# Kernel tuning notes

Measured on AMD Instinct MI355X. Metric: run time of the kernel, lower is better.

## Reference

```python
import jax, jax.numpy as jnp
import numpy as np

IN_SHAPE = 640
LEVELS = [3, 4, 5]          # pyramid_levels [3,5] expanded
REG_LEN = 64
NUM_CLASSES = 80
MAX_OUT = 100
SCORE_TH = 0.3
IOU_TH = 0.5
NEG_INF = -1e30


def _make_anchors():
    """Anchor-free anchors: one box per grid cell, grid_zero_start=True,
    anchor_scale=1, aspect_ratio=1 -> half-size = stride/2. Normalized by input size."""
    all_a = []
    for lvl in LEVELS:
        stride = 2 ** lvl
        fs = IN_SHAPE // stride
        hh = np.arange(fs, dtype='float32') * stride
        ww = np.arange(fs, dtype='float32') * stride
        wg, hg = np.meshgrid(ww, hh)
        centers = np.stack([hg, wg], -1).reshape(-1, 2)  # [fs*fs, 2] (h, w)
        half = stride * 0.5
        all_a.append(np.concatenate([centers - half, centers + half], -1))
    return np.concatenate(all_a, 0) / IN_SHAPE  # [8400, 4]


def setup_inputs() -> dict:
    key = jax.random.key(0)
    preds = jax.random.normal(key, (64, 8400, REG_LEN + NUM_CLASSES), dtype=jnp.float32)
    anchors = jnp.asarray(_make_anchors(), dtype=jnp.float32)
    return {"preds": preds, "anchors": anchors}


def _decode_yolov8(preds, anchors):
    bbox_logits, cls_logits = preds[..., :REG_LEN], preds[..., REG_LEN:]
    B, N = bbox_logits.shape[:2]
    bins = REG_LEN // 4  # 16
    d = bbox_logits.reshape(B, N, 4, bins)
    # softmax-weighted DFL expectation over bins
    d = jnp.sum(jax.nn.softmax(d, axis=-1) * jnp.arange(bins, dtype=d.dtype), axis=-1)  # [B,N,4]
    tl, br = d[..., :2], d[..., 2:]
    anchors_hw = anchors[:, 2:] - anchors[:, :2]          # [N,2]
    anchors_ctr = (anchors[:, :2] + anchors[:, 2:]) * 0.5  # [N,2]
    bc = (br - tl) * 0.5 * anchors_hw + anchors_ctr        # center
    bhw = (br + tl) * anchors_hw                           # height/width
    boxes = jnp.concatenate([bc - bhw * 0.5, bc + bhw * 0.5], -1)  # [B,N,4] corners
    return boxes, cls_logits


def _iou_one_vs_all(box, boxes):
    tl = jnp.maximum(box[:2], boxes[:, :2])
    br = jnp.minimum(box[2:], boxes[:, 2:])
    inter = jnp.prod(jnp.clip(br - tl, 0.0, None), -1)
    a1 = jnp.prod(box[2:] - box[:2])
    a2 = jnp.prod(boxes[:, 2:] - boxes[:, :2], -1)
    return inter / (a1 + a2 - inter + 1e-9)


def _nms_single(boxes, scores):
    """Greedy hard NMS for one image. boxes [N,4], scores [N] -> idxs [MAX_OUT] (-1 = invalid)."""
    n = scores.shape[0]
    sc0 = jnp.where(scores > SCORE_TH, scores, NEG_INF)

    def step(sc, _):
        j = jnp.argmax(sc)
        valid = sc[j] > NEG_INF * 0.5
        idx = jnp.where(valid, j, -1).astype(jnp.int32)
        iou = _iou_one_vs_all(boxes[j], boxes)
        sc = jnp.where((iou > IOU_TH) | (jnp.arange(n) == j), NEG_INF, sc)
        return sc, idx

    _, idxs = jax.lax.scan(step, sc0, None, length=MAX_OUT)
    return idxs


def reference(preds, anchors):
    boxes, cls = _decode_yolov8(preds, anchors)       # [B,N,4], [B,N,C]
    scores = jnp.max(cls, -1)                          # [B,N]
    labels = jnp.argmax(cls, -1).astype(jnp.int32)     # [B,N]
    idxs = jax.vmap(_nms_single)(boxes, scores)        # [B,MAX_OUT]
    valid = idxs >= 0
    safe = jnp.maximum(idxs, 0)
    out_boxes = jnp.take_along_axis(boxes, safe[:, :, None], axis=1) * valid[..., None]
    out_scores = jnp.take_along_axis(scores, safe, axis=1) * valid
    out_labels = jnp.where(valid, jnp.take_along_axis(labels, safe, axis=1), -1)
    return out_boxes, out_labels, out_scores
```

## Files before the change

### kernel.cpp

```cpp
#include <hip/hip_runtime.h>

namespace {
constexpr int kB = 64;
constexpr int kN = 8400;
constexpr int kMain = 8192;
constexpr int kTail = kN - kMain;
constexpr int kReg = 64;
constexpr int kCls = 80;
constexpr int kStride = kReg + kCls;
constexpr int kMaxOut = 100;
constexpr float kScoreTh = 0.3f;
constexpr float kIouTh = 0.5f;
}

__global__ __launch_bounds__(256) void decode2_k(
    const float* __restrict__ preds,
    const float* __restrict__ anchors,
    float4* __restrict__ boxes,
    float* __restrict__ scores,
    int* __restrict__ labels,
    unsigned long long* __restrict__ keys)
{
    __shared__ float lds[64 * 148];
    const int tid = threadIdx.x;
    const size_t gbase = (size_t)blockIdx.x * 64;

    const float4* src = (const float4*)(preds + gbase * kStride);
    float4* l4 = (float4*)lds;
#pragma unroll
    for (int k = 0; k < 9; ++k) {
        int i = tid + k * 256;
        int row = i / 36, col = i - row * 36;
        l4[row * 37 + col] = src[i];
    }
    __syncthreads();

    const int a = tid >> 2, s = tid & 3;
    const float* rowp = lds + a * 148;

    float x[16];
    const float4* q = (const float4*)(rowp + s * 16);
#pragma unroll
    for (int j = 0; j < 4; ++j) ((float4*)x)[j] = q[j];
    float m = x[0];
#pragma unroll
    for (int j = 1; j < 16; ++j) m = fmaxf(m, x[j]);
    float se = 0.f, we = 0.f;
#pragma unroll
    for (int j = 0; j < 16; ++j) {
        float t = expf(x[j] - m);
        se += t;
        we += t * (float)j;
    }
    float d = we / se;

    const float4* cl = (const float4*)(rowp + kReg + s * 20);
    float bv = -3e38f; int bi = 0;
#pragma unroll
    for (int c = 0; c < 5; ++c) {
        float4 v = cl[c];
        int cb = s * 20 + 4 * c;
        if (v.x > bv) { bv = v.x; bi = cb; }
        if (v.y > bv) { bv = v.y; bi = cb + 1; }
        if (v.z > bv) { bv = v.z; bi = cb + 2; }
        if (v.w > bv) { bv = v.w; bi = cb + 3; }
    }

    const int lane = tid & 63;
    const int base = lane & ~3;
    float d0 = __shfl(d, base + 0, 64);
    float d1 = __shfl(d, base + 1, 64);
    float d2 = __shfl(d, base + 2, 64);
    float d3 = __shfl(d, base + 3, 64);
    float v1 = __shfl(bv, base + 1, 64); int i1 = __shfl(bi, base + 1, 64);
    float v2 = __shfl(bv, base + 2, 64); int i2 = __shfl(bi, base + 2, 64);
    float v3 = __shfl(bv, base + 3, 64); int i3 = __shfl(bi, base + 3, 64);

    if (s == 0) {
        float best = bv; int bl = bi;
        if (v1 > best) { best = v1; bl = i1; }
        if (v2 > best) { best = v2; bl = i2; }
        if (v3 > best) { best = v3; bl = i3; }

        size_t gi = gbase + a;
        int bimg = (int)(gi / kN);
        int n = (int)(gi - (size_t)bimg * kN);
        float4 av = ((const float4*)anchors)[n];
        float ah0 = av.z - av.x, ah1 = av.w - av.y;
        float c0 = (av.x + av.z) * 0.5f, c1 = (av.y + av.w) * 0.5f;
        float bc0 = (d2 - d0) * 0.5f * ah0 + c0;
        float bc1 = (d3 - d1) * 0.5f * ah1 + c1;
        float bh0 = (d2 + d0) * ah0;
        float bh1 = (d3 + d1) * ah1;
        boxes[gi] = make_float4(bc0 - bh0 * 0.5f, bc1 - bh1 * 0.5f,
                                bc0 + bh0 * 0.5f, bc1 + bh1 * 0.5f);
        scores[gi] = best;
        labels[gi] = bl;

        unsigned long long kkey = ~0ULL;
        if (best > kScoreTh) {
            unsigned u = __float_as_uint(best);
            unsigned o = u ^ ((u & 0x80000000u) ? 0xFFFFFFFFu : 0x80000000u);
            kkey = ((unsigned long long)(~o) << 32) | (unsigned)n;
        }
        keys[((size_t)bimg << 14) + n] = kkey;
    }
}

__global__ __launch_bounds__(512) void sortL_k(unsigned long long* __restrict__ keys)
{
    __shared__ unsigned long long lk[2048];
    const int tid = threadIdx.x;
    const int img = blockIdx.x >> 2, seg = blockIdx.x & 3;
    const int gofs = seg << 11;
    unsigned long long* base = keys + ((size_t)img << 14) + gofs;

    unsigned long long r[4];
    const int e0 = tid << 2;
#pragma unroll
    for (int k = 0; k < 4; ++k) r[k] = base[e0 + k];

    auto ce2 = [&](int size) {
#pragma unroll
        for (int k = 0; k < 2; ++k) {
            bool desc = (((gofs + e0 + k) & size) != 0);
            unsigned long long a = r[k], c = r[k + 2];
            bool sw = desc ? (c > a) : (a > c);
            if (sw) { r[k] = c; r[k + 2] = a; }
        }
    };
    auto ce1 = [&](int size) {
#pragma unroll
        for (int k = 0; k < 4; k += 2) {
            bool desc = (((gofs + e0 + k) & size) != 0);
            unsigned long long a = r[k], c = r[k + 1];
            bool sw = desc ? (c > a) : (a > c);
            if (sw) { r[k] = c; r[k + 1] = a; }
        }
    };

    ce1(2);
    for (int size = 4; size <= 2048; size <<= 1) {
        for (int stride = size >> 1; stride >= 4; stride >>= 1) {
            if (stride >= 256) {
                __syncthreads();
#pragma unroll
                for (int k = 0; k < 4; ++k) lk[k * 512 + tid] = r[k];
                __syncthreads();
                const int pt = tid ^ (stride >> 2);
#pragma unroll
                for (int k = 0; k < 4; ++k) {
                    unsigned long long o = lk[k * 512 + pt];
                    int e = e0 + k;
                    bool keep_min = (((e & stride) == 0) !=
                                     (((gofs + e) & size) != 0));
                    r[k] = keep_min ? (r[k] < o ? r[k] : o)
                                    : (r[k] > o ? r[k] : o);
                }
            } else {
                const int d = stride >> 2;
#pragma unroll
                for (int k = 0; k < 4; ++k) {
                    unsigned long long o = __shfl_xor(r[k], d, 64);
                    int e = e0 + k;
                    bool keep_min = (((e & stride) == 0) !=
                                     (((gofs + e) & size) != 0));
                    r[k] = keep_min ? (r[k] < o ? r[k] : o)
                                    : (r[k] > o ? r[k] : o);
                }
            }
        }
        ce2(size);
        ce1(size);
    }
#pragma unroll
    for (int k = 0; k < 4; ++k) base[e0 + k] = r[k];
}

__global__ __launch_bounds__(256) void gce_k(unsigned long long* __restrict__ keys)
{
    int tg = blockIdx.x * 256 + threadIdx.x;
    int img = tg >> 12;
    int n = tg & 4095;
    unsigned long long* base = keys + ((size_t)img << 14);
    unsigned long long a = base[n], c = base[n + 4096];
    if (a > c) { base[n] = c; base[n + 4096] = a; }
}

template <int SIZE>
__global__ __launch_bounds__(512) void lm2_k(unsigned long long* __restrict__ keys)
{
    __shared__ unsigned long long lk[4096];
    const int tid = threadIdx.x;
    const int img = blockIdx.x >> 1, half = blockIdx.x & 1;
    const int gofs = half << 12;
    unsigned long long* base = keys + ((size_t)img << 14) + gofs;
    const bool desc = (gofs & SIZE) != 0;

    unsigned long long r[8];
    const int e0 = tid << 3;
#pragma unroll
    for (int k = 0; k < 8; ++k) r[k] = base[e0 + k];

    for (int stride = 2048; stride >= 512; stride >>= 1) {
        __syncthreads();
#pragma unroll
        for (int k = 0; k < 8; ++k) lk[k * 512 + tid] = r[k];
        __syncthreads();
        const int pt = tid ^ (stride >> 3);
#pragma unroll
        for (int k = 0; k < 8; ++k) {
            unsigned long long o = lk[k * 512 + pt];
            bool keep_min = ((((e0 + k) & stride) == 0) != desc);
            r[k] = keep_min ? (r[k] < o ? r[k] : o) : (r[k] > o ? r[k] : o);
        }
    }
    for (int stride = 256; stride >= 8; stride >>= 1) {
        const int d = stride >> 3;
#pragma unroll
        for (int k = 0; k < 8; ++k) {
            unsigned long long o = __shfl_xor(r[k], d, 64);
            bool keep_min = ((((e0 + k) & stride) == 0) != desc);
            r[k] = keep_min ? (r[k] < o ? r[k] : o) : (r[k] > o ? r[k] : o);
        }
    }
    auto ce = [&](int i, int j) {
        unsigned long long a = r[i], c = r[j];
        bool sw = desc ? (c > a) : (a > c);
        if (sw) { r[i] = c; r[j] = a; }
    };
    ce(0, 4); ce(1, 5); ce(2, 6); ce(3, 7);
    ce(0, 2); ce(1, 3); ce(4, 6); ce(5, 7);
    ce(0, 1); ce(2, 3); ce(4, 5); ce(6, 7);
#pragma unroll
    for (int k = 0; k < 8; ++k) base[e0 + k] = r[k];
}

__device__ __forceinline__ unsigned long long getB_(
    const unsigned long long* tailL, int p1, int x)
{
    int t = p1 + x;
    return (t < 256) ? tailL[t] : ~0ULL;
}

__global__ __launch_bounds__(256) void nms_k(
    const float4* __restrict__ boxes,
    const float* __restrict__ scores,
    const int* __restrict__ labels,
    const unsigned long long* __restrict__ keys,
    float* __restrict__ out)
{
    __shared__ unsigned long long tailL[256];
    __shared__ unsigned long long aw[512];
    __shared__ float4 sbox[256];
    __shared__ float  sar[256];
    __shared__ int    sidx[256];
    __shared__ float4 kboxL[kMaxOut];
    __shared__ float  kareaL[kMaxOut];
    __shared__ int    kidxL[kMaxOut];
    __shared__ unsigned long long ballS[4];
    __shared__ int p0S, p1S, kcS, doneS, stopS;

    const int b = blockIdx.x, tid = threadIdx.x;
    const unsigned long long* mainA = keys + ((size_t)b << 14);
    const float4* bx = boxes + (size_t)b * kN;

    if (tid == 0) { p0S = 0; p1S = 0; kcS = 0; doneS = 0; }

    tailL[tid] = (tid < kTail) ? mainA[kMain + tid] : ~0ULL;
    __syncthreads();
    for (int size = 2; size <= 256; size <<= 1) {
        for (int stride = size >> 1; stride > 0; stride >>= 1) {
            if (tid < 128) {
                int i = ((tid & ~(stride - 1)) << 1) | (tid & (stride - 1));
                int j = i + stride;
                bool desc = (i & size) != 0;
                unsigned long long a = tailL[i], c = tailL[j];
                bool sw = desc ? (c > a) : (a > c);
                if (sw) { tailL[i] = c; tailL[j] = a; }
            }
            __syncthreads();
        }
    }

    int kc = 0;
    for (int c = 0; c < 33; ++c) {
        int p0 = p0S, p1 = p1S;
        aw[tid]       = (p0 + tid       < kMain) ? mainA[p0 + tid]       : ~0ULL;
        aw[tid + 256] = (p0 + tid + 256 < kMain) ? mainA[p0 + tid + 256] : ~0ULL;
        __syncthreads();

        int d = tid;
        int lo = 0, hi = d;
        while (lo < hi) {
            int mid = (lo + hi) >> 1;
            bool c2 = getB_(tailL, p1, d - mid - 1) < aw[mid];
            if (c2) hi = mid; else lo = mid + 1;
        }
        unsigned long long av = aw[lo];
        unsigned long long bv = getB_(tailL, p1, d - lo);
        unsigned long long key = (av <= bv) ? av : bv;

        bool alive = (key != ~0ULL);
        int idx = alive ? (int)(key & 0xFFFFFFFFULL) : 0;
        float4 cb = bx[idx];
        float ac = (cb.z - cb.x) * (cb.w - cb.y);

        if (alive) {
            for (int k = 0; k < kc; ++k) {
                float4 kb = kboxL[k];
                float t0 = fmaxf(kb.x, cb.x), t1 = fmaxf(kb.y, cb.y);
                float b0 = fminf(kb.z, cb.z), b1 = fminf(kb.w, cb.w);
                float inter = fmaxf(b0 - t0, 0.f) * fmaxf(b1 - t1, 0.f);
                float iou = inter / (kareaL[k] + ac - inter + 1e-9f);
                if (iou > kIouTh) { alive = false; break; }
            }
        }
        sbox[tid] = cb; sar[tid] = ac; sidx[tid] = idx;
        unsigned long long mm = __ballot((int)alive);
        if ((tid & 63) == 0) ballS[tid >> 6] = mm;
        if (tid == 0) {
            stopS = (key == ~0ULL);
            int lo2 = 0, hi2 = 256;
            while (lo2 < hi2) {
                int mid = (lo2 + hi2) >> 1;
                bool c2 = getB_(tailL, p1, 255 - mid) < aw[mid];
                if (c2) hi2 = mid; else lo2 = mid + 1;
            }
            p0S = p0 + lo2; p1S = p1 + (256 - lo2);
        }
        __syncthreads();
        if (stopS) break;

        if (tid < 64) {
            const int lane = tid;
            unsigned a4 = 0;
#pragma unroll
            for (int j = 0; j < 4; ++j)
                a4 |= (unsigned)((ballS[j] >> lane) & 1ULL) << j;
            int kcl = kc;
            while (true) {
                int jF = -1, lF = 0;
#pragma unroll
                for (int j = 0; j < 4; ++j) {
                    if (jF < 0) {
                        unsigned long long m2 = __ballot((int)((a4 >> j) & 1u));
                        if (m2) { jF = j; lF = __ffsll((unsigned long long)m2) - 1; }
                    }
                }
                if (jF < 0) break;
                int cs = (jF << 6) + lF;
                float4 kb = sbox[cs];
                float kar = sar[cs];
                if (lane == 0) {
                    kboxL[kcl] = kb; kareaL[kcl] = kar; kidxL[kcl] = sidx[cs];
                }
                if (lane == lF) a4 &= ~(1u << jF);
                ++kcl;
                if (kcl == kMaxOut) break;
#pragma unroll
                for (int j = 0; j < 4; ++j) {
                    if ((a4 >> j) & 1u) {
                        float4 cb2 = sbox[lane + (j << 6)];
                        float ac2 = sar[lane + (j << 6)];
                        float t0 = fmaxf(kb.x, cb2.x), t1 = fmaxf(kb.y, cb2.y);
                        float b0 = fminf(kb.z, cb2.z), b1 = fminf(kb.w, cb2.w);
                        float inter = fmaxf(b0 - t0, 0.f) * fmaxf(b1 - t1, 0.f);
                        float iou = inter / (kar + ac2 - inter + 1e-9f);
                        if (iou > kIouTh) a4 &= ~(1u << j);
                    }
                }
            }
            if (lane == 0) { kcS = kcl; if (kcl == kMaxOut) doneS = 1; }
        }
        __syncthreads();
        kc = kcS;
        if (doneS) break;
    }

    int kcf = kcS;
    if (tid < kMaxOut) {
        if (tid < kcf) {
            int idx = kidxL[tid];
            ((float4*)out)[b * kMaxOut + tid] = kboxL[tid];
            out[kB * kMaxOut * 4 + b * kMaxOut + tid] =
                (float)labels[(size_t)b * kN + idx];
            out[kB * kMaxOut * 5 + b * kMaxOut + tid] =
                scores[(size_t)b * kN + idx];
        } else {
            ((float4*)out)[b * kMaxOut + tid] = make_float4(0.f, 0.f, 0.f, 0.f);
            out[kB * kMaxOut * 4 + b * kMaxOut + tid] = -1.0f;
            out[kB * kMaxOut * 5 + b * kMaxOut + tid] = 0.0f;
        }
    }
}

extern "C" void kernel_launch(void* const* d_in, const int* in_sizes, int n_in,
                              void* d_out, int out_size, void* d_ws, size_t ws_size,
                              hipStream_t stream)
{
    const float* preds = (const float*)d_in[0];
    const float* anchors = (const float*)d_in[1];
    float* out = (float*)d_out;

    char* ws = (char*)d_ws;
    float4* boxes = (float4*)ws;
    float* scores = (float*)(ws + (size_t)kB * kN * 16);
    int* labels = (int*)(ws + (size_t)kB * kN * 20);
    unsigned long long* keys =
        (unsigned long long*)(ws + (size_t)kB * kN * 24);

    decode2_k<<<(kB * kN) / 64, 256, 0, stream>>>(preds, anchors, boxes, scores, labels, keys);
    sortL_k<<<kB * 4, 512, 0, stream>>>(keys);
    lm2_k<4096><<<kB * 2, 512, 0, stream>>>(keys);
    gce_k<<<(kB * 4096) / 256, 256, 0, stream>>>(keys);
    lm2_k<8192><<<kB * 2, 512, 0, stream>>>(keys);
    nms_k<<<kB, 256, 0, stream>>>(boxes, scores, labels, keys, out);
}
```

Measured before the change: 509.3 us.

## Fuse final bitonic merge stages into NMS kernel using LDS-resident sorted keys

Removes the three separate merge kernels (two lm2_k launches and gce_k) and performs the final 4096- and 8192-size bitonic merge stages inside the NMS kernel with 512 threads holding 16 keys each. The sorted main keys stay in shared memory, so the NMS candidate window reads them from LDS instead of global memory. This cuts launches and global round trips but runs the merge on only 64 blocks, leaving much of the GPU idle, and the 64KB of LDS plus 16 keys per thread in registers may limit occupancy.

```diff
diff --git a/kernel.cpp b/kernel.cpp
--- a/kernel.cpp
+++ b/kernel.cpp
@@ -177,65 +177,6 @@
     for (int k = 0; k < 4; ++k) base[e0 + k] = r[k];
 }
 
-__global__ __launch_bounds__(256) void gce_k(unsigned long long* __restrict__ keys)
-{
-    int tg = blockIdx.x * 256 + threadIdx.x;
-    int img = tg >> 12;
-    int n = tg & 4095;
-    unsigned long long* base = keys + ((size_t)img << 14);
-    unsigned long long a = base[n], c = base[n + 4096];
-    if (a > c) { base[n] = c; base[n + 4096] = a; }
-}
-
-template <int SIZE>
-__global__ __launch_bounds__(512) void lm2_k(unsigned long long* __restrict__ keys)
-{
-    __shared__ unsigned long long lk[4096];
-    const int tid = threadIdx.x;
-    const int img = blockIdx.x >> 1, half = blockIdx.x & 1;
-    const int gofs = half << 12;
-    unsigned long long* base = keys + ((size_t)img << 14) + gofs;
-    const bool desc = (gofs & SIZE) != 0;
-
-    unsigned long long r[8];
-    const int e0 = tid << 3;
-#pragma unroll
-    for (int k = 0; k < 8; ++k) r[k] = base[e0 + k];
-
-    for (int stride = 2048; stride >= 512; stride >>= 1) {
-        __syncthreads();
-#pragma unroll
-        for (int k = 0; k < 8; ++k) lk[k * 512 + tid] = r[k];
-        __syncthreads();
-        const int pt = tid ^ (stride >> 3);
-#pragma unroll
-        for (int k = 0; k < 8; ++k) {
-            unsigned long long o = lk[k * 512 + pt];
-            bool keep_min = ((((e0 + k) & stride) == 0) != desc);
-            r[k] = keep_min ? (r[k] < o ? r[k] : o) : (r[k] > o ? r[k] : o);
-        }
-    }
-    for (int stride = 256; stride >= 8; stride >>= 1) {
-        const int d = stride >> 3;
-#pragma unroll
-        for (int k = 0; k < 8; ++k) {
-            unsigned long long o = __shfl_xor(r[k], d, 64);
-            bool keep_min = ((((e0 + k) & stride) == 0) != desc);
-            r[k] = keep_min ? (r[k] < o ? r[k] : o) : (r[k] > o ? r[k] : o);
-        }
-    }
-    auto ce = [&](int i, int j) {
-        unsigned long long a = r[i], c = r[j];
-        bool sw = desc ? (c > a) : (a > c);
-        if (sw) { r[i] = c; r[j] = a; }
-    };
-    ce(0, 4); ce(1, 5); ce(2, 6); ce(3, 7);
-    ce(0, 2); ce(1, 3); ce(4, 6); ce(5, 7);
-    ce(0, 1); ce(2, 3); ce(4, 5); ce(6, 7);
-#pragma unroll
-    for (int k = 0; k < 8; ++k) base[e0 + k] = r[k];
-}
-
 __device__ __forceinline__ unsigned long long getB_(
     const unsigned long long* tailL, int p1, int x)
 {
@@ -243,15 +184,15 @@
     return (t < 256) ? tailL[t] : ~0ULL;
 }
 
-__global__ __launch_bounds__(256) void nms_k(
+__global__ __launch_bounds__(512) void snms_k(
     const float4* __restrict__ boxes,
     const float* __restrict__ scores,
     const int* __restrict__ labels,
     const unsigned long long* __restrict__ keys,
     float* __restrict__ out)
 {
+    __shared__ unsigned long long lk[8192];
     __shared__ unsigned long long tailL[256];
-    __shared__ unsigned long long aw[512];
     __shared__ float4 sbox[256];
     __shared__ float  sar[256];
     __shared__ int    sidx[256];
@@ -262,13 +203,59 @@
     __shared__ int p0S, p1S, kcS, doneS, stopS;
 
     const int b = blockIdx.x, tid = threadIdx.x;
-    const unsigned long long* mainA = keys + ((size_t)b << 14);
+    const unsigned long long* mainG = keys + ((size_t)b << 14);
     const float4* bx = boxes + (size_t)b * kN;
 
+    unsigned long long r[16];
+    const int e0 = tid << 4;
+#pragma unroll
+    for (int k = 0; k < 16; ++k) r[k] = mainG[e0 + k];
+
+    for (int size = 4096; size <= 8192; size <<= 1) {
+        const bool desc = (e0 & size) != 0;
+        for (int stride = size >> 1; stride >= 1024; stride >>= 1) {
+            __syncthreads();
+#pragma unroll
+            for (int k = 0; k < 16; ++k) lk[k * 512 + tid] = r[k];
+            __syncthreads();
+            const int pt = tid ^ (stride >> 4);
+            const bool keep_min = ((e0 & stride) == 0) != desc;
+#pragma unroll
+            for (int k = 0; k < 16; ++k) {
+                unsigned long long o = lk[k * 512 + pt];
+                r[k] = keep_min ? (r[k] < o ? r[k] : o)
+                                : (r[k] > o ? r[k] : o);
+            }
+        }
+        for (int stride = 512; stride >= 16; stride >>= 1) {
+            const int d = stride >> 4;
+            const bool keep_min = ((e0 & stride) == 0) != desc;
+#pragma unroll
+            for (int k = 0; k < 16; ++k) {
+                unsigned long long o = __shfl_xor(r[k], d, 64);
+                r[k] = keep_min ? (r[k] < o ? r[k] : o)
+                                : (r[k] > o ? r[k] : o);
+            }
+        }
+        auto ce = [&](int i, int j) {
+            unsigned long long a = r[i], c = r[j];
+            bool sw = desc ? (c > a) : (a > c);
+            if (sw) { r[i] = c; r[j] = a; }
+        };
+        ce(0,8); ce(1,9); ce(2,10); ce(3,11); ce(4,12); ce(5,13); ce(6,14); ce(7,15);
+        ce(0,4); ce(1,5); ce(2,6); ce(3,7); ce(8,12); ce(9,13); ce(10,14); ce(11,15);
+        ce(0,2); ce(1,3); ce(4,6); ce(5,7); ce(8,10); ce(9,11); ce(12,14); ce(13,15);
+        ce(0,1); ce(2,3); ce(4,5); ce(6,7); ce(8,9); ce(10,11); ce(12,13); ce(14,15);
+    }
+    __syncthreads();
+#pragma unroll
+    for (int k = 0; k < 16; ++k) lk[e0 + k] = r[k];
+
     if (tid == 0) { p0S = 0; p1S = 0; kcS = 0; doneS = 0; }
-
-    tailL[tid] = (tid < kTail) ? mainA[kMain + tid] : ~0ULL;
+    if (tid < 256)
+        tailL[tid] = (tid < kTail) ? mainG[kMain + tid] : ~0ULL;
     __syncthreads();
+
     for (int size = 2; size <= 256; size <<= 1) {
         for (int stride = size >> 1; stride > 0; stride >>= 1) {
             if (tid < 128) {
@@ -286,46 +273,48 @@
     int kc = 0;
     for (int c = 0; c < 33; ++c) {
         int p0 = p0S, p1 = p1S;
-        aw[tid]       = (p0 + tid       < kMain) ? mainA[p0 + tid]       : ~0ULL;
-        aw[tid + 256] = (p0 + tid + 256 < kMain) ? mainA[p0 + tid + 256] : ~0ULL;
-        __syncthreads();
-
-        int d = tid;
-        int lo = 0, hi = d;
-        while (lo < hi) {
-            int mid = (lo + hi) >> 1;
-            bool c2 = getB_(tailL, p1, d - mid - 1) < aw[mid];
-            if (c2) hi = mid; else lo = mid + 1;
-        }
-        unsigned long long av = aw[lo];
-        unsigned long long bv = getB_(tailL, p1, d - lo);
-        unsigned long long key = (av <= bv) ? av : bv;
-
-        bool alive = (key != ~0ULL);
-        int idx = alive ? (int)(key & 0xFFFFFFFFULL) : 0;
-        float4 cb = bx[idx];
-        float ac = (cb.z - cb.x) * (cb.w - cb.y);
-
-        if (alive) {
-            for (int k = 0; k < kc; ++k) {
-                float4 kb = kboxL[k];
-                float t0 = fmaxf(kb.x, cb.x), t1 = fmaxf(kb.y, cb.y);
-                float b0 = fminf(kb.z, cb.z), b1 = fminf(kb.w, cb.w);
-                float inter = fmaxf(b0 - t0, 0.f) * fmaxf(b1 - t1, 0.f);
-                float iou = inter / (kareaL[k] + ac - inter + 1e-9f);
-                if (iou > kIouTh) { alive = false; break; }
-            }
-        }
-        sbox[tid] = cb; sar[tid] = ac; sidx[tid] = idx;
-        unsigned long long mm = __ballot((int)alive);
-        if ((tid & 63) == 0) ballS[tid >> 6] = mm;
+        unsigned long long key = ~0ULL;
+        if (tid < 256) {
+            int dd = tid, lo = 0, hi = dd;
+            while (lo < hi) {
+                int mid = (lo + hi) >> 1;
+                unsigned long long amid =
+                    (p0 + mid < kMain) ? lk[p0 + mid] : ~0ULL;
+                if (getB_(tailL, p1, dd - mid - 1) < amid) hi = mid;
+                else lo = mid + 1;
+            }
+            unsigned long long av = (p0 + lo < kMain) ? lk[p0 + lo] : ~0ULL;
+            unsigned long long bv = getB_(tailL, p1, dd - lo);
+            key = (av <= bv) ? av : bv;
+
+            bool alive = (key != ~0ULL);
+            int idx = alive ? (int)(key & 0xFFFFFFFFULL) : 0;
+            float4 cb = bx[idx];
+            float ac = (cb.z - cb.x) * (cb.w - cb.y);
+
+            if (alive) {
+                for (int k = 0; k < kc; ++k) {
+                    float4 kb = kboxL[k];
+                    float t0 = fmaxf(kb.x, cb.x), t1 = fmaxf(kb.y, cb.y);
+                    float b0 = fminf(kb.z, cb.z), b1 = fminf(kb.w, cb.w);
+                    float inter = fmaxf(b0 - t0, 0.f) * fmaxf(b1 - t1, 0.f);
+                    float iou = inter / (kareaL[k] + ac - inter + 1e-9f);
+                    if (iou > kIouTh) { alive = false; break; }
+                }
+            }
+            sbox[tid] = cb; sar[tid] = ac; sidx[tid] = idx;
+            unsigned long long mm = __ballot((int)alive);
+            if ((tid & 63) == 0) ballS[tid >> 6] = mm;
+        }
         if (tid == 0) {
             stopS = (key == ~0ULL);
             int lo2 = 0, hi2 = 256;
             while (lo2 < hi2) {
                 int mid = (lo2 + hi2) >> 1;
-                bool c2 = getB_(tailL, p1, 255 - mid) < aw[mid];
-                if (c2) hi2 = mid; else lo2 = mid + 1;
+                unsigned long long amid =
+                    (p0 + mid < kMain) ? lk[p0 + mid] : ~0ULL;
+                if (getB_(tailL, p1, 255 - mid) < amid) hi2 = mid;
+                else lo2 = mid + 1;
             }
             p0S = p0 + lo2; p1S = p1 + (256 - lo2);
         }
@@ -412,8 +401,5 @@
 
     decode2_k<<<(kB * kN) / 64, 256, 0, stream>>>(preds, anchors, boxes, scores, labels, keys);
     sortL_k<<<kB * 4, 512, 0, stream>>>(keys);
-    lm2_k<4096><<<kB * 2, 512, 0, stream>>>(keys);
-    gce_k<<<(kB * 4096) / 256, 256, 0, stream>>>(keys);
-    lm2_k<8192><<<kB * 2, 512, 0, stream>>>(keys);
-    nms_k<<<kB, 256, 0, stream>>>(boxes, scores, labels, keys, out);
-}
+    snms_k<<<kB, 512, 0, stream>>>(boxes, scores, labels, keys, out);
+}
```

Measured after the change: 508.4 us. No clear change (-0.2%).
